# Kernel tuning notes

Measured on AMD Instinct MI355X. Metric: run time of the kernel, lower is better.

## Reference

```python
import jax, jax.numpy as jnp
import numpy as np

N_NODES = 100000
N_EDGES = 625000
D_IN = 128
D_OUT = 128


def setup_inputs() -> dict:
    key = jax.random.key(0)
    k1, k2, k3, k4, k5 = jax.random.split(key, 5)
    scale = 1.0 / np.sqrt(D_IN)
    x = jax.random.normal(k1, (N_NODES, D_IN), dtype=jnp.float32)
    edge_index = jax.random.randint(k2, (2, N_EDGES), 0, N_NODES, dtype=jnp.int64)
    W_l = jax.random.normal(k3, (D_IN, D_OUT), dtype=jnp.float32) * scale
    b_l = jax.random.normal(k4, (D_OUT,), dtype=jnp.float32) * scale
    W_r = jax.random.normal(k5, (D_IN, D_OUT), dtype=jnp.float32) * scale
    return {"x": x, "edge_index": edge_index, "W_l": W_l, "b_l": b_l, "W_r": W_r}


def reference(x, edge_index, W_l, b_l, W_r):
    # SAGEConv (mean aggr, no self loops):
    #   out = lin_l(mean_{j in N(i)} x_j) + lin_r(x_i)
    src = edge_index[0]  # message source nodes
    dst = edge_index[1]  # aggregation targets
    n = x.shape[0]
    msgs = x[src]  # [E, D_IN] gather
    agg = jax.ops.segment_sum(msgs, dst, num_segments=n)  # [N, D_IN]
    deg = jax.ops.segment_sum(jnp.ones_like(dst, dtype=x.dtype), dst, num_segments=n)
    mean = agg / jnp.maximum(deg, 1.0)[:, None]  # isolated nodes -> 0
    return mean @ W_l + b_l + x @ W_r
```

## Files before the change

kernel.cpp:

```cpp
#include <hip/hip_runtime.h>


constexpr int N_NODES = 100000;
constexpr int N_EDGES = 625000;
constexpr int D = 128;
constexpr int SCAN_CHUNK = 1024;
constexpr int N_SCAN_BLOCKS = (N_NODES + SCAN_CHUNK - 1) / SCAN_CHUNK;

typedef __attribute__((ext_vector_type(8))) short short8;
typedef __attribute__((ext_vector_type(4))) short short4v;
typedef __attribute__((ext_vector_type(4))) float f32x4;

__device__ __forceinline__ unsigned short f2bf(float f) {
    union { float f; unsigned int u; } c; c.f = f;
    unsigned int u = c.u + 0x7fffu + ((c.u >> 16) & 1u);
    return (unsigned short)(u >> 16);
}
__device__ __forceinline__ float bflo(unsigned int v) {
    union { unsigned int u; float f; } c; c.u = v << 16; return c.f;
}
__device__ __forceinline__ float bfhi(unsigned int v) {
    union { unsigned int u; float f; } c; c.u = v & 0xffff0000u; return c.f;
}

__global__ __launch_bounds__(256) void csr_hist(
    const int* __restrict__ dst, int* __restrict__ cnt)
{
    int e = blockIdx.x * 256 + threadIdx.x;
    if (e < N_EDGES) atomicAdd(&cnt[dst[e]], 1);
}

__global__ __launch_bounds__(256) void scan_blocks(
    const int* __restrict__ cnt, int* __restrict__ ptr, int* __restrict__ bsums)
{
    __shared__ int sh[256];
    const int t = threadIdx.x;
    const int base = blockIdx.x * SCAN_CHUNK + t * 4;
    int v0 = (base + 0 < N_NODES) ? cnt[base + 0] : 0;
    int v1 = (base + 1 < N_NODES) ? cnt[base + 1] : 0;
    int v2 = (base + 2 < N_NODES) ? cnt[base + 2] : 0;
    int v3 = (base + 3 < N_NODES) ? cnt[base + 3] : 0;
    const int tsum = v0 + v1 + v2 + v3;
    sh[t] = tsum;
    __syncthreads();
    #pragma unroll
    for (int off = 1; off < 256; off <<= 1) {
        int val = (t >= off) ? sh[t - off] : 0;
        __syncthreads();
        sh[t] += val;
        __syncthreads();
    }
    const int texcl = sh[t] - tsum;
    if (t == 255) bsums[blockIdx.x] = sh[255];
    int e0 = texcl, e1 = e0 + v0, e2 = e1 + v1, e3 = e2 + v2;
    if (base + 0 < N_NODES) ptr[base + 0] = e0;
    if (base + 1 < N_NODES) ptr[base + 1] = e1;
    if (base + 2 < N_NODES) ptr[base + 2] = e2;
    if (base + 3 < N_NODES) ptr[base + 3] = e3;
}

__global__ __launch_bounds__(128) void scan_bsums(int* __restrict__ bsums)
{
    __shared__ int sh[128];
    const int t = threadIdx.x;
    int v = (t < N_SCAN_BLOCKS) ? bsums[t] : 0;
    sh[t] = v;
    __syncthreads();
    #pragma unroll
    for (int off = 1; off < 128; off <<= 1) {
        int val = (t >= off) ? sh[t - off] : 0;
        __syncthreads();
        sh[t] += val;
        __syncthreads();
    }
    if (t < N_SCAN_BLOCKS) bsums[t] = sh[t] - v;
}

__global__ __launch_bounds__(256) void add_offsets(
    int* __restrict__ ptr, int* __restrict__ cursor, const int* __restrict__ bsums)
{
    int i = blockIdx.x * 256 + threadIdx.x;
    if (i < N_NODES) {
        int p = ptr[i] + bsums[i >> 10];
        ptr[i] = p;
        cursor[i] = p;
    }
    if (i == 0) ptr[N_NODES] = N_EDGES;
}

__global__ __launch_bounds__(256) void csr_fill(
    const int* __restrict__ src, const int* __restrict__ dst,
    int* __restrict__ cursor, int* __restrict__ sorted_src)
{
    int e = blockIdx.x * 256 + threadIdx.x;
    if (e < N_EDGES) {
        int t = dst[e];
        int pos = atomicAdd(&cursor[t], 1);
        sorted_src[pos] = src[e];
    }
}

__global__ __launch_bounds__(256) void x2bf(
    const float* __restrict__ x, unsigned short* __restrict__ xb)
{
    int c = blockIdx.x * 256 + threadIdx.x;
    if (c >= N_NODES * D / 8) return;
    const float4* xp = (const float4*)x;
    float4 a = xp[(size_t)c * 2];
    float4 b = xp[(size_t)c * 2 + 1];
    short8 v;
    v[0] = (short)f2bf(a.x); v[1] = (short)f2bf(a.y);
    v[2] = (short)f2bf(a.z); v[3] = (short)f2bf(a.w);
    v[4] = (short)f2bf(b.x); v[5] = (short)f2bf(b.y);
    v[6] = (short)f2bf(b.z); v[7] = (short)f2bf(b.w);
    ((short8*)xb)[c] = v;
}

__global__ __launch_bounds__(256) void wt_build(
    const float* __restrict__ Wl, const float* __restrict__ Wr,
    unsigned short* __restrict__ wT)
{
    int idx = blockIdx.x * 256 + threadIdx.x;
    if (idx >= 128 * 256) return;
    int n = idx >> 8;
    int k = idx & 255;
    float v = (k < 128) ? Wl[k * 128 + n] : Wr[(k - 128) * 128 + n];
    wT[n * 256 + k] = f2bf(v);
}

template<bool MBF>
__global__ __launch_bounds__(256) void sage_aggregate_bf(
    const unsigned short* __restrict__ xb,
    const int* __restrict__ ptr,
    const int* __restrict__ sorted_src,
    unsigned short* __restrict__ mean_bf,
    float* __restrict__ mean_f32)
{
    const int node = blockIdx.x * 4 + (threadIdx.x >> 6);
    if (node >= N_NODES) return;
    const int lane = threadIdx.x & 63;
    const int beg = ptr[node];
    const int end = ptr[node + 1];
    const int off = lane * 2;

    float a0 = 0.f, a1 = 0.f, b0 = 0.f, b1 = 0.f;
    float c0 = 0.f, c1 = 0.f, d0 = 0.f, d1 = 0.f;
    int i = beg;
    for (; i + 3 < end; i += 4) {
        int s0 = sorted_src[i], s1 = sorted_src[i + 1];
        int s2 = sorted_src[i + 2], s3 = sorted_src[i + 3];
        unsigned int v0 = *(const unsigned int*)&xb[(size_t)s0 * D + off];
        unsigned int v1 = *(const unsigned int*)&xb[(size_t)s1 * D + off];
        unsigned int v2 = *(const unsigned int*)&xb[(size_t)s2 * D + off];
        unsigned int v3 = *(const unsigned int*)&xb[(size_t)s3 * D + off];
        a0 += bflo(v0); a1 += bfhi(v0);
        b0 += bflo(v1); b1 += bfhi(v1);
        c0 += bflo(v2); c1 += bfhi(v2);
        d0 += bflo(v3); d1 += bfhi(v3);
    }
    for (; i < end; ++i) {
        int s0 = sorted_src[i];
        unsigned int v0 = *(const unsigned int*)&xb[(size_t)s0 * D + off];
        a0 += bflo(v0); a1 += bfhi(v0);
    }
    const float sc = 1.0f / fmaxf((float)(end - beg), 1.0f);
    float r0 = ((a0 + b0) + (c0 + d0)) * sc;
    float r1 = ((a1 + b1) + (c1 + d1)) * sc;
    if (MBF) {
        unsigned int r = (unsigned int)f2bf(r0) | ((unsigned int)f2bf(r1) << 16);
        *(unsigned int*)&mean_bf[(size_t)node * D + off] = r;
    } else {
        *(float2*)&mean_f32[(size_t)node * D + off] = make_float2(r0, r1);
    }
}

template<bool MBF>
__global__ __launch_bounds__(256) void sage_gemm_bf(
    const unsigned short* __restrict__ xb,
    const unsigned short* __restrict__ mean_bf,
    const unsigned short* __restrict__ wT,
    const float* __restrict__ bl,
    float* __restrict__ out)
{
    __shared__ unsigned short sW[128 * 256];
    __shared__ unsigned short sA[32 * 256];

    const int tid  = threadIdx.x;
    const int lane = tid & 63;
    const int w    = tid >> 6;
    const int l15  = lane & 15;
    const int lg   = lane >> 4;

    #pragma unroll
    for (int i = 0; i < 16; ++i) {
        int c  = tid + i * 256;
        int n  = c >> 5;
        int k8 = c & 31;
        short8 v = ((const short8*)wT)[c];
        *(short8*)&sW[n * 256 + ((k8 ^ (n & 7)) << 3)] = v;
    }

    const int a_r0 = l15;
    const int a_r1 = 16 + l15;
    const int n0 = w * 32 + l15;
    const int n1 = n0 + 16;
    const float bias0 = bl[n0];
    const float bias1 = bl[n1];

    const int nTiles = N_NODES / 32;

    for (int tile = blockIdx.x; tile < nTiles; tile += gridDim.x) {
        const int row0 = tile * 32;

        if constexpr (MBF) {
            #pragma unroll
            for (int i = 0; i < 4; ++i) {
                int c = tid + i * 256;
                int r = c >> 5;
                int s = c & 31;
                const unsigned short* srcp = (s < 16)
                    ? &mean_bf[(size_t)(row0 + r) * D + s * 8]
                    : &xb[(size_t)(row0 + r) * D + (s - 16) * 8];
                short8 v = *(const short8*)srcp;
                *(short8*)&sA[r * 256 + ((s ^ (r & 7)) << 3)] = v;
            }
        } else {
            #pragma unroll
            for (int i = 0; i < 4; ++i) {
                int c = tid + i * 256;
                int r = c >> 5;
                int f4 = c & 31;
                float4 v = *(const float4*)&out[(size_t)(row0 + r) * D + f4 * 4];
                short4v b;
                b.x = (short)f2bf(v.x); b.y = (short)f2bf(v.y);
                b.z = (short)f2bf(v.z); b.w = (short)f2bf(v.w);
                int u = f4 >> 1;
                *(short4v*)&sA[r * 256 + ((u ^ (r & 7)) << 3) + (f4 & 1) * 4] = b;
            }
            #pragma unroll
            for (int i = 0; i < 2; ++i) {
                int c = tid + i * 256;
                int r = c >> 4;
                int s = 16 + (c & 15);
                short8 v = *(const short8*)&xb[(size_t)(row0 + r) * D + (c & 15) * 8];
                *(short8*)&sA[r * 256 + ((s ^ (r & 7)) << 3)] = v;
            }
        }
        __syncthreads();

        f32x4 acc00 = {0.f,0.f,0.f,0.f}, acc01 = {0.f,0.f,0.f,0.f};
        f32x4 acc10 = {0.f,0.f,0.f,0.f}, acc11 = {0.f,0.f,0.f,0.f};

        #pragma unroll
        for (int s = 0; s < 8; ++s) {
            int ks = s * 4 + lg;
            short8 a0 = *(const short8*)&sA[a_r0 * 256 + ((ks ^ (a_r0 & 7)) << 3)];
            short8 a1 = *(const short8*)&sA[a_r1 * 256 + ((ks ^ (a_r1 & 7)) << 3)];
            short8 b0 = *(const short8*)&sW[n0 * 256 + ((ks ^ (n0 & 7)) << 3)];
            short8 b1 = *(const short8*)&sW[n1 * 256 + ((ks ^ (n1 & 7)) << 3)];
            acc00 = __builtin_amdgcn_mfma_f32_16x16x32_bf16(a0, b0, acc00, 0, 0, 0);
            acc01 = __builtin_amdgcn_mfma_f32_16x16x32_bf16(a0, b1, acc01, 0, 0, 0);
            acc10 = __builtin_amdgcn_mfma_f32_16x16x32_bf16(a1, b0, acc10, 0, 0, 0);
            acc11 = __builtin_amdgcn_mfma_f32_16x16x32_bf16(a1, b1, acc11, 0, 0, 0);
        }
        __syncthreads();

        #pragma unroll
        for (int reg = 0; reg < 4; ++reg) {
            int r0w = row0 + lg * 4 + reg;
            int r1w = r0w + 16;
            out[(size_t)r0w * D + n0] = acc00[reg] + bias0;
            out[(size_t)r0w * D + n1] = acc01[reg] + bias1;
            out[(size_t)r1w * D + n0] = acc10[reg] + bias0;
            out[(size_t)r1w * D + n1] = acc11[reg] + bias1;
        }
    }
}

__global__ __launch_bounds__(256) void sage_aggregate(
    const float* __restrict__ x,
    const int* __restrict__ ptr,
    const int* __restrict__ sorted_src,
    float* __restrict__ mean)
{
    const int node = blockIdx.x * 4 + (threadIdx.x >> 6);
    if (node >= N_NODES) return;
    const int lane = threadIdx.x & 63;
    const int beg = ptr[node];
    const int end = ptr[node + 1];

    float2 acc0 = make_float2(0.f, 0.f);
    float2 acc1 = make_float2(0.f, 0.f);
    int i = beg;
    for (; i + 1 < end; i += 2) {
        int s0 = sorted_src[i];
        int s1 = sorted_src[i + 1];
        float2 a = *(const float2*)&x[(size_t)s0 * D + lane * 2];
        float2 b = *(const float2*)&x[(size_t)s1 * D + lane * 2];
        acc0.x += a.x; acc0.y += a.y;
        acc1.x += b.x; acc1.y += b.y;
    }
    if (i < end) {
        int s0 = sorted_src[i];
        float2 a = *(const float2*)&x[(size_t)s0 * D + lane * 2];
        acc0.x += a.x; acc0.y += a.y;
    }
    const float sc = 1.0f / fmaxf((float)(end - beg), 1.0f);
    float2 r = make_float2((acc0.x + acc1.x) * sc, (acc0.y + acc1.y) * sc);
    *(float2*)&mean[(size_t)node * D + lane * 2] = r;
}

__global__ __launch_bounds__(256) void sage_gemm_mfma(
    const float* __restrict__ x,
    const unsigned short* __restrict__ wT,
    const float* __restrict__ bl,
    float* __restrict__ out)
{
    __shared__ unsigned short sW[128 * 256];
    __shared__ unsigned short sA[32 * 256];

    const int tid  = threadIdx.x;
    const int lane = tid & 63;
    const int w    = tid >> 6;
    const int l15  = lane & 15;
    const int lg   = lane >> 4;

    #pragma unroll
    for (int i = 0; i < 16; ++i) {
        int c  = tid + i * 256;
        int n  = c >> 5;
        int k8 = c & 31;
        short8 v = ((const short8*)wT)[c];
        *(short8*)&sW[n * 256 + ((k8 ^ (n & 7)) << 3)] = v;
    }

    const int a_r0 = l15;
    const int a_r1 = 16 + l15;
    const int n0 = w * 32 + l15;
    const int n1 = n0 + 16;
    const float bias0 = bl[n0];
    const float bias1 = bl[n1];
    const int nTiles = N_NODES / 32;

    for (int tile = blockIdx.x; tile < nTiles; tile += gridDim.x) {
        const int row0 = tile * 32;
        #pragma unroll
        for (int i = 0; i < 8; ++i) {
            int c    = tid + i * 256;
            int r    = c >> 6;
            int half = (c >> 5) & 1;
            int f4   = c & 31;
            const float* srcp = half ? &x[(size_t)(row0 + r) * D + f4 * 4]
                                     : &out[(size_t)(row0 + r) * D + f4 * 4];
            float4 v = *(const float4*)srcp;
            short4v b;
            b.x = (short)f2bf(v.x); b.y = (short)f2bf(v.y);
            b.z = (short)f2bf(v.z); b.w = (short)f2bf(v.w);
            int k = half * 128 + f4 * 4;
            int u = k >> 3;
            *(short4v*)&sA[r * 256 + ((u ^ (r & 7)) << 3) + (k & 7)] = b;
        }
        __syncthreads();

        f32x4 acc00 = {0.f,0.f,0.f,0.f}, acc01 = {0.f,0.f,0.f,0.f};
        f32x4 acc10 = {0.f,0.f,0.f,0.f}, acc11 = {0.f,0.f,0.f,0.f};

        #pragma unroll
        for (int s = 0; s < 8; ++s) {
            int ks = s * 4 + lg;
            short8 a0 = *(const short8*)&sA[a_r0 * 256 + ((ks ^ (a_r0 & 7)) << 3)];
            short8 a1 = *(const short8*)&sA[a_r1 * 256 + ((ks ^ (a_r1 & 7)) << 3)];
            short8 b0 = *(const short8*)&sW[n0 * 256 + ((ks ^ (n0 & 7)) << 3)];
            short8 b1 = *(const short8*)&sW[n1 * 256 + ((ks ^ (n1 & 7)) << 3)];
            acc00 = __builtin_amdgcn_mfma_f32_16x16x32_bf16(a0, b0, acc00, 0, 0, 0);
            acc01 = __builtin_amdgcn_mfma_f32_16x16x32_bf16(a0, b1, acc01, 0, 0, 0);
            acc10 = __builtin_amdgcn_mfma_f32_16x16x32_bf16(a1, b0, acc10, 0, 0, 0);
            acc11 = __builtin_amdgcn_mfma_f32_16x16x32_bf16(a1, b1, acc11, 0, 0, 0);
        }
        __syncthreads();

        #pragma unroll
        for (int reg = 0; reg < 4; ++reg) {
            int r0w = row0 + lg * 4 + reg;
            int r1w = r0w + 16;
            out[(size_t)r0w * D + n0] = acc00[reg] + bias0;
            out[(size_t)r0w * D + n1] = acc01[reg] + bias1;
            out[(size_t)r1w * D + n0] = acc10[reg] + bias0;
            out[(size_t)r1w * D + n1] = acc11[reg] + bias1;
        }
    }
}

__global__ __launch_bounds__(256) void sage_scatter(
    const float* __restrict__ x, const int* __restrict__ src,
    const int* __restrict__ dst, float* __restrict__ agg, float* __restrict__ deg)
{
    int gid = blockIdx.x * 256 + threadIdx.x;
    int e = gid >> 7;
    if (e >= N_EDGES) return;
    int d = gid & 127;
    atomicAdd(&agg[(size_t)dst[e] * D + d], x[(size_t)src[e] * D + d]);
    if (d == 0) atomicAdd(&deg[dst[e]], 1.0f);
}

__global__ __launch_bounds__(256) void apply_mean(
    float* __restrict__ agg, const float* __restrict__ deg)
{
    int gid = blockIdx.x * 256 + threadIdx.x;
    int row = gid >> 5;
    if (row >= N_NODES) return;
    float sc = 1.0f / fmaxf(deg[row], 1.0f);
    float4 v = ((float4*)agg)[gid];
    v.x *= sc; v.y *= sc; v.z *= sc; v.w *= sc;
    ((float4*)agg)[gid] = v;
}

__device__ __forceinline__ void accum_tile(
    float acc[4][4], const float (*sWf)[D], const float (*srow)[D], int h, int j4)
{
    #pragma unroll 2
    for (int k = 0; k < D; k += 4) {
        float4 w0 = *(const float4*)&sWf[k + 0][j4];
        float4 w1 = *(const float4*)&sWf[k + 1][j4];
        float4 w2 = *(const float4*)&sWf[k + 2][j4];
        float4 w3 = *(const float4*)&sWf[k + 3][j4];
        #pragma unroll
        for (int r = 0; r < 4; ++r) {
            float4 a = *(const float4*)&srow[h + r * 8][k];
            acc[r][0] = fmaf(a.x, w0.x, fmaf(a.y, w1.x, fmaf(a.z, w2.x, fmaf(a.w, w3.x, acc[r][0]))));
            acc[r][1] = fmaf(a.x, w0.y, fmaf(a.y, w1.y, fmaf(a.z, w2.y, fmaf(a.w, w3.y, acc[r][1]))));
            acc[r][2] = fmaf(a.x, w0.z, fmaf(a.y, w1.z, fmaf(a.z, w2.z, fmaf(a.w, w3.z, acc[r][2]))));
            acc[r][3] = fmaf(a.x, w0.w, fmaf(a.y, w1.w, fmaf(a.z, w2.w, fmaf(a.w, w3.w, acc[r][3]))));
        }
    }
}

__global__ __launch_bounds__(256) void sage_gemm_f32(
    const float* __restrict__ x, const float* __restrict__ Wl,
    const float* __restrict__ bl, const float* __restrict__ Wr,
    float* __restrict__ out)
{
    __shared__ float sWf[D][D];
    __shared__ float srow[32][D];
    const int tid = threadIdx.x;
    const int j4 = (tid & 31) * 4;
    const int h  = tid >> 5;
    const int nTiles = (N_NODES + 31) / 32;
    const float4 bias = *(const float4*)(bl + j4);

    for (int tile = blockIdx.x; tile < nTiles; tile += gridDim.x) {
        const int row0 = tile * 32;
        float acc[4][4];
        #pragma unroll
        for (int r = 0; r < 4; ++r)
            #pragma unroll
            for (int c = 0; c < 4; ++c) acc[r][c] = 0.0f;

        __syncthreads();
        #pragma unroll
        for (int i = 0; i < 16; ++i)
            ((float4*)sWf)[tid + i * 256] = ((const float4*)Wl)[tid + i * 256];
        #pragma unroll
        for (int i = 0; i < 4; ++i) {
            int idx = tid + i * 256, r = idx >> 5, c = idx & 31, row = row0 + r;
            float4 v = make_float4(0.f,0.f,0.f,0.f);
            if (row < N_NODES) v = ((const float4*)out)[(size_t)row * 32 + c];
            ((float4*)srow)[idx] = v;
        }
        __syncthreads();
        accum_tile(acc, sWf, srow, h, j4);

        __syncthreads();
        #pragma unroll
        for (int i = 0; i < 16; ++i)
            ((float4*)sWf)[tid + i * 256] = ((const float4*)Wr)[tid + i * 256];
        #pragma unroll
        for (int i = 0; i < 4; ++i) {
            int idx = tid + i * 256, r = idx >> 5, c = idx & 31, row = row0 + r;
            float4 v = make_float4(0.f,0.f,0.f,0.f);
            if (row < N_NODES) v = ((const float4*)x)[(size_t)row * 32 + c];
            ((float4*)srow)[idx] = v;
        }
        __syncthreads();
        accum_tile(acc, sWf, srow, h, j4);

        #pragma unroll
        for (int r = 0; r < 4; ++r) {
            int row = row0 + h + r * 8;
            if (row < N_NODES) {
                float4 v = make_float4(acc[r][0] + bias.x, acc[r][1] + bias.y,
                                       acc[r][2] + bias.z, acc[r][3] + bias.w);
                *(float4*)(out + (size_t)row * D + j4) = v;
            }
        }
    }
}

extern "C" void kernel_launch(void* const* d_in, const int* in_sizes, int n_in,
                              void* d_out, int out_size, void* d_ws, size_t ws_size,
                              hipStream_t stream) {
    const float* x   = (const float*)d_in[0];
    const int*   ei  = (const int*)d_in[1];
    const float* Wl  = (const float*)d_in[2];
    const float* bl  = (const float*)d_in[3];
    const float* Wr  = (const float*)d_in[4];
    float* out = (float*)d_out;

    const int* src = ei;
    const int* dst = ei + N_EDGES;

    int* cnt    = (int*)d_ws;
    int* ptr    = cnt + N_NODES;
    int* cursor = ptr + N_NODES + 1;
    int* bsums  = cursor + N_NODES;
    int* sorted = bsums + 128;
    unsigned short* xb      = (unsigned short*)(sorted + N_EDGES);
    unsigned short* mean_bf = xb + (size_t)N_NODES * D;

    size_t base_ints = (size_t)(3 * N_NODES + 1 + 128 + N_EDGES);
    size_t need_B  = base_ints * sizeof(int);
    size_t need_A2 = need_B + (size_t)N_NODES * D * 2;
    size_t need_A  = need_A2 + (size_t)N_NODES * D * 2;

    if (ws_size >= need_B) {
        hipMemsetAsync(cnt, 0, (size_t)N_NODES * sizeof(int), stream);
        csr_hist<<<(N_EDGES + 255) / 256, 256, 0, stream>>>(dst, cnt);
        scan_blocks<<<N_SCAN_BLOCKS, 256, 0, stream>>>(cnt, ptr, bsums);
        scan_bsums<<<1, 128, 0, stream>>>(bsums);
        add_offsets<<<(N_NODES + 255) / 256, 256, 0, stream>>>(ptr, cursor, bsums);
        csr_fill<<<(N_EDGES + 255) / 256, 256, 0, stream>>>(src, dst, cursor, sorted);

        unsigned short* wT = (unsigned short*)cursor;
        wt_build<<<(128 * 256 + 255) / 256, 256, 0, stream>>>(Wl, Wr, wT);

        if (ws_size >= need_A) {
            x2bf<<<(N_NODES * D / 8 + 255) / 256, 256, 0, stream>>>(x, xb);
            sage_aggregate_bf<true><<<(N_NODES + 3) / 4, 256, 0, stream>>>(
                xb, ptr, sorted, mean_bf, nullptr);
            sage_gemm_bf<true><<<512, 256, 0, stream>>>(xb, mean_bf, wT, bl, out);
        } else if (ws_size >= need_A2) {
            x2bf<<<(N_NODES * D / 8 + 255) / 256, 256, 0, stream>>>(x, xb);
            sage_aggregate_bf<false><<<(N_NODES + 3) / 4, 256, 0, stream>>>(
                xb, ptr, sorted, nullptr, out);
            sage_gemm_bf<false><<<512, 256, 0, stream>>>(xb, nullptr, wT, bl, out);
        } else {
            sage_aggregate<<<(N_NODES + 3) / 4, 256, 0, stream>>>(x, ptr, sorted, out);
            sage_gemm_mfma<<<512, 256, 0, stream>>>(x, wT, bl, out);
        }
    } else {
        float* deg = (float*)d_ws;
        hipMemsetAsync(out, 0, (size_t)N_NODES * D * sizeof(float), stream);
        hipMemsetAsync(deg, 0, (size_t)N_NODES * sizeof(float), stream);
        long long total = (long long)N_EDGES * 128;
        sage_scatter<<<(int)((total + 255) / 256), 256, 0, stream>>>(x, src, dst, out, deg);
        apply_mean<<<(N_NODES * 32 + 255) / 256, 256, 0, stream>>>(out, deg);
        sage_gemm_f32<<<512, 256, 0, stream>>>(x, Wl, bl, Wr, out);
    }
}
```

Before: 154.2 us.

## Fuse scan offset kernels, merge weight prep into x conversion, widen aggregate loads

Replaces the separate block-sum scan and offset-add kernels with one kernel where each block reduces the preceding block sums itself. Folds the transposed weight build into the x-to-bf16 conversion kernel and moves wT to its own workspace slot. The aggregation kernel now uses 16 lanes per node with 16-byte loads instead of 64 lanes with 4-byte loads, giving four nodes per wave and fewer load instructions. Together these cut kernel launches and improve gather efficiency, at the cost of more registers per thread and a slightly larger workspace requirement.

```diff
diff --git a/kernel.cpp b/kernel.cpp
--- a/kernel.cpp
+++ b/kernel.cpp
@@ -59,33 +59,31 @@
     if (base + 3 < N_NODES) ptr[base + 3] = e3;
 }
 
-__global__ __launch_bounds__(128) void scan_bsums(int* __restrict__ bsums)
-{
-    __shared__ int sh[128];
+__global__ __launch_bounds__(256) void add_offsets_fused(
+    int* __restrict__ ptr, int* __restrict__ cursor, const int* __restrict__ bsums)
+{
+    __shared__ int sh[256];
     const int t = threadIdx.x;
-    int v = (t < N_SCAN_BLOCKS) ? bsums[t] : 0;
+    int v = (t < blockIdx.x) ? bsums[t] : 0;
     sh[t] = v;
     __syncthreads();
     #pragma unroll
-    for (int off = 1; off < 128; off <<= 1) {
-        int val = (t >= off) ? sh[t - off] : 0;
-        __syncthreads();
-        sh[t] += val;
-        __syncthreads();
-    }
-    if (t < N_SCAN_BLOCKS) bsums[t] = sh[t] - v;
-}
-
-__global__ __launch_bounds__(256) void add_offsets(
-    int* __restrict__ ptr, int* __restrict__ cursor, const int* __restrict__ bsums)
-{
-    int i = blockIdx.x * 256 + threadIdx.x;
-    if (i < N_NODES) {
-        int p = ptr[i] + bsums[i >> 10];
-        ptr[i] = p;
-        cursor[i] = p;
-    }
-    if (i == 0) ptr[N_NODES] = N_EDGES;
+    for (int off = 128; off > 0; off >>= 1) {
+        if (t < off) sh[t] += sh[t + off];
+        __syncthreads();
+    }
+    const int soff = sh[0];
+    const int base = blockIdx.x * SCAN_CHUNK + t * 4;
+    #pragma unroll
+    for (int j = 0; j < 4; ++j) {
+        int i = base + j;
+        if (i < N_NODES) {
+            int p = ptr[i] + soff;
+            ptr[i] = p;
+            cursor[i] = p;
+        }
+    }
+    if (blockIdx.x == 0 && t == 0) ptr[N_NODES] = N_EDGES;
 }
 
 __global__ __launch_bounds__(256) void csr_fill(
@@ -100,20 +98,36 @@
     }
 }
 
-__global__ __launch_bounds__(256) void x2bf(
-    const float* __restrict__ x, unsigned short* __restrict__ xb)
-{
+__global__ __launch_bounds__(256) void prep_bf(
+    const float* __restrict__ x, const float* __restrict__ Wl,
+    const float* __restrict__ Wr,
+    unsigned short* __restrict__ xb, unsigned short* __restrict__ wT)
+{
+    const int XC = N_NODES * D / 8;
     int c = blockIdx.x * 256 + threadIdx.x;
-    if (c >= N_NODES * D / 8) return;
-    const float4* xp = (const float4*)x;
-    float4 a = xp[(size_t)c * 2];
-    float4 b = xp[(size_t)c * 2 + 1];
-    short8 v;
-    v[0] = (short)f2bf(a.x); v[1] = (short)f2bf(a.y);
-    v[2] = (short)f2bf(a.z); v[3] = (short)f2bf(a.w);
-    v[4] = (short)f2bf(b.x); v[5] = (short)f2bf(b.y);
-    v[6] = (short)f2bf(b.z); v[7] = (short)f2bf(b.w);
-    ((short8*)xb)[c] = v;
+    if (c < XC) {
+        const float4* xp = (const float4*)x;
+        float4 a = xp[(size_t)c * 2];
+        float4 b = xp[(size_t)c * 2 + 1];
+        short8 v;
+        v[0] = (short)f2bf(a.x); v[1] = (short)f2bf(a.y);
+        v[2] = (short)f2bf(a.z); v[3] = (short)f2bf(a.w);
+        v[4] = (short)f2bf(b.x); v[5] = (short)f2bf(b.y);
+        v[6] = (short)f2bf(b.z); v[7] = (short)f2bf(b.w);
+        ((short8*)xb)[c] = v;
+    } else if (c < XC + 4096) {
+        int idx = c - XC;
+        int n  = idx >> 5;
+        int k0 = (idx & 31) * 8;
+        short8 v;
+        #pragma unroll
+        for (int j = 0; j < 8; ++j) {
+            int k = k0 + j;
+            float f = (k < 128) ? Wl[k * 128 + n] : Wr[(k - 128) * 128 + n];
+            v[j] = (short)f2bf(f);
+        }
+        *(short8*)&wT[n * 256 + k0] = v;
+    }
 }
 
 __global__ __launch_bounds__(256) void wt_build(
@@ -136,41 +150,57 @@
     unsigned short* __restrict__ mean_bf,
     float* __restrict__ mean_f32)
 {
-    const int node = blockIdx.x * 4 + (threadIdx.x >> 6);
+    const int node = blockIdx.x * 16 + (threadIdx.x >> 4);
     if (node >= N_NODES) return;
-    const int lane = threadIdx.x & 63;
+    const int l = threadIdx.x & 15;
     const int beg = ptr[node];
     const int end = ptr[node + 1];
-    const int off = lane * 2;
-
-    float a0 = 0.f, a1 = 0.f, b0 = 0.f, b1 = 0.f;
-    float c0 = 0.f, c1 = 0.f, d0 = 0.f, d1 = 0.f;
+    const size_t off = (size_t)l * 8;
+
+    float a0=0,a1=0,a2=0,a3=0,a4=0,a5=0,a6=0,a7=0;
+    float b0=0,b1=0,b2=0,b3=0,b4=0,b5=0,b6=0,b7=0;
+    float c0=0,c1=0,c2=0,c3=0,c4=0,c5=0,c6=0,c7=0;
+    float d0=0,d1=0,d2=0,d3=0,d4=0,d5=0,d6=0,d7=0;
+
     int i = beg;
     for (; i + 3 < end; i += 4) {
-        int s0 = sorted_src[i], s1 = sorted_src[i + 1];
+        int s0 = sorted_src[i],     s1 = sorted_src[i + 1];
         int s2 = sorted_src[i + 2], s3 = sorted_src[i + 3];
-        unsigned int v0 = *(const unsigned int*)&xb[(size_t)s0 * D + off];
-        unsigned int v1 = *(const unsigned int*)&xb[(size_t)s1 * D + off];
-        unsigned int v2 = *(const unsigned int*)&xb[(size_t)s2 * D + off];
-        unsigned int v3 = *(const unsigned int*)&xb[(size_t)s3 * D + off];
-        a0 += bflo(v0); a1 += bfhi(v0);
-        b0 += bflo(v1); b1 += bfhi(v1);
-        c0 += bflo(v2); c1 += bfhi(v2);
-        d0 += bflo(v3); d1 += bfhi(v3);
+        uint4 v0 = *(const uint4*)&xb[(size_t)s0 * D + off];
+        uint4 v1 = *(const uint4*)&xb[(size_t)s1 * D + off];
+        uint4 v2 = *(const uint4*)&xb[(size_t)s2 * D + off];
+        uint4 v3 = *(const uint4*)&xb[(size_t)s3 * D + off];
+        a0+=bflo(v0.x); a1+=bfhi(v0.x); a2+=bflo(v0.y); a3+=bfhi(v0.y);
+        a4+=bflo(v0.z); a5+=bfhi(v0.z); a6+=bflo(v0.w); a7+=bfhi(v0.w);
+        b0+=bflo(v1.x); b1+=bfhi(v1.x); b2+=bflo(v1.y); b3+=bfhi(v1.y);
+        b4+=bflo(v1.z); b5+=bfhi(v1.z); b6+=bflo(v1.w); b7+=bfhi(v1.w);
+        c0+=bflo(v2.x); c1+=bfhi(v2.x); c2+=bflo(v2.y); c3+=bfhi(v2.y);
+        c4+=bflo(v2.z); c5+=bfhi(v2.z); c6+=bflo(v2.w); c7+=bfhi(v2.w);
+        d0+=bflo(v3.x); d1+=bfhi(v3.x); d2+=bflo(v3.y); d3+=bfhi(v3.y);
+        d4+=bflo(v3.z); d5+=bfhi(v3.z); d6+=bflo(v3.w); d7+=bfhi(v3.w);
     }
     for (; i < end; ++i) {
         int s0 = sorted_src[i];
-        unsigned int v0 = *(const unsigned int*)&xb[(size_t)s0 * D + off];
-        a0 += bflo(v0); a1 += bfhi(v0);
+        uint4 v0 = *(const uint4*)&xb[(size_t)s0 * D + off];
+        a0+=bflo(v0.x); a1+=bfhi(v0.x); a2+=bflo(v0.y); a3+=bfhi(v0.y);
+        a4+=bflo(v0.z); a5+=bfhi(v0.z); a6+=bflo(v0.w); a7+=bfhi(v0.w);
     }
     const float sc = 1.0f / fmaxf((float)(end - beg), 1.0f);
-    float r0 = ((a0 + b0) + (c0 + d0)) * sc;
-    float r1 = ((a1 + b1) + (c1 + d1)) * sc;
-    if (MBF) {
-        unsigned int r = (unsigned int)f2bf(r0) | ((unsigned int)f2bf(r1) << 16);
-        *(unsigned int*)&mean_bf[(size_t)node * D + off] = r;
+    float r0 = ((a0+b0)+(c0+d0))*sc, r1 = ((a1+b1)+(c1+d1))*sc;
+    float r2 = ((a2+b2)+(c2+d2))*sc, r3 = ((a3+b3)+(c3+d3))*sc;
+    float r4 = ((a4+b4)+(c4+d4))*sc, r5 = ((a5+b5)+(c5+d5))*sc;
+    float r6 = ((a6+b6)+(c6+d6))*sc, r7 = ((a7+b7)+(c7+d7))*sc;
+
+    if constexpr (MBF) {
+        uint4 o;
+        o.x = (unsigned)f2bf(r0) | ((unsigned)f2bf(r1) << 16);
+        o.y = (unsigned)f2bf(r2) | ((unsigned)f2bf(r3) << 16);
+        o.z = (unsigned)f2bf(r4) | ((unsigned)f2bf(r5) << 16);
+        o.w = (unsigned)f2bf(r6) | ((unsigned)f2bf(r7) << 16);
+        *(uint4*)&mean_bf[(size_t)node * D + off] = o;
     } else {
-        *(float2*)&mean_f32[(size_t)node * D + off] = make_float2(r0, r1);
+        *(float4*)&mean_f32[(size_t)node * D + off] = make_float4(r0, r1, r2, r3);
+        *(float4*)&mean_f32[(size_t)node * D + off + 4] = make_float4(r4, r5, r6, r7);
     }
 }
 
@@ -514,38 +544,37 @@
     int* cursor = ptr + N_NODES + 1;
     int* bsums  = cursor + N_NODES;
     int* sorted = bsums + 128;
-    unsigned short* xb      = (unsigned short*)(sorted + N_EDGES);
+    unsigned short* wT      = (unsigned short*)(sorted + N_EDGES);
+    unsigned short* xb      = wT + 128 * 256;
     unsigned short* mean_bf = xb + (size_t)N_NODES * D;
 
     size_t base_ints = (size_t)(3 * N_NODES + 1 + 128 + N_EDGES);
     size_t need_B  = base_ints * sizeof(int);
-    size_t need_A2 = need_B + (size_t)N_NODES * D * 2;
+    size_t need_A2 = need_B + 128 * 256 * 2 + (size_t)N_NODES * D * 2;
     size_t need_A  = need_A2 + (size_t)N_NODES * D * 2;
 
     if (ws_size >= need_B) {
         hipMemsetAsync(cnt, 0, (size_t)N_NODES * sizeof(int), stream);
         csr_hist<<<(N_EDGES + 255) / 256, 256, 0, stream>>>(dst, cnt);
         scan_blocks<<<N_SCAN_BLOCKS, 256, 0, stream>>>(cnt, ptr, bsums);
-        scan_bsums<<<1, 128, 0, stream>>>(bsums);
-        add_offsets<<<(N_NODES + 255) / 256, 256, 0, stream>>>(ptr, cursor, bsums);
+        add_offsets_fused<<<N_SCAN_BLOCKS, 256, 0, stream>>>(ptr, cursor, bsums);
         csr_fill<<<(N_EDGES + 255) / 256, 256, 0, stream>>>(src, dst, cursor, sorted);
 
-        unsigned short* wT = (unsigned short*)cursor;
-        wt_build<<<(128 * 256 + 255) / 256, 256, 0, stream>>>(Wl, Wr, wT);
-
         if (ws_size >= need_A) {
-            x2bf<<<(N_NODES * D / 8 + 255) / 256, 256, 0, stream>>>(x, xb);
-            sage_aggregate_bf<true><<<(N_NODES + 3) / 4, 256, 0, stream>>>(
+            prep_bf<<<(N_NODES * D / 8 + 4096 + 255) / 256, 256, 0, stream>>>(x, Wl, Wr, xb, wT);
+            sage_aggregate_bf<true><<<(N_NODES + 15) / 16, 256, 0, stream>>>(
                 xb, ptr, sorted, mean_bf, nullptr);
             sage_gemm_bf<true><<<512, 256, 0, stream>>>(xb, mean_bf, wT, bl, out);
         } else if (ws_size >= need_A2) {
-            x2bf<<<(N_NODES * D / 8 + 255) / 256, 256, 0, stream>>>(x, xb);
-            sage_aggregate_bf<false><<<(N_NODES + 3) / 4, 256, 0, stream>>>(
+            prep_bf<<<(N_NODES * D / 8 + 4096 + 255) / 256, 256, 0, stream>>>(x, Wl, Wr, xb, wT);
+            sage_aggregate_bf<false><<<(N_NODES + 15) / 16, 256, 0, stream>>>(
                 xb, ptr, sorted, nullptr, out);
             sage_gemm_bf<false><<<512, 256, 0, stream>>>(xb, nullptr, wT, bl, out);
         } else {
+            unsigned short* wTc = (unsigned short*)cursor;
+            wt_build<<<(128 * 256 + 255) / 256, 256, 0, stream>>>(Wl, Wr, wTc);
             sage_aggregate<<<(N_NODES + 3) / 4, 256, 0, stream>>>(x, ptr, sorted, out);
-            sage_gemm_mfma<<<512, 256, 0, stream>>>(x, wT, bl, out);
+            sage_gemm_mfma<<<512, 256, 0, stream>>>(x, wTc, bl, out);
         }
     } else {
         float* deg = (float*)d_ws;
```

Measured after the change: 144.9 us. 6.1% less time.
